# Performance work log

Hardware: AMD Instinct MI355X
Metric: run time of the kernel (lower is better)

Reference implementation:

```python
import jax, jax.numpy as jnp
import numpy as np

H = 32          # query heads
HKV = 8         # kv heads
HD = 128        # head dim
BS = 64         # sparse block size
LOCAL = 16      # local blocks
VERT = 8        # vertical stride
STEP = 1        # head sliding step = max(1, VERT // H) for non-homo heads
BASE = 1000000.0
ROPE_SCALE = 1.0
SCALE = 1.0 / np.sqrt(HD)


def setup_inputs() -> dict:
    key = jax.random.key(0)
    ks = jax.random.split(key, 6)
    T, D = 2048, H * HD
    std = 0.02
    return {
        'hidden_states': jax.random.normal(ks[0], (T, D), jnp.float32),
        'positions': jnp.arange(T, dtype=jnp.int32),
        'Wq': jax.random.normal(ks[1], (D, H * HD), jnp.float32) * std,
        'bq': jnp.zeros((H * HD,), jnp.float32),
        'Wk': jax.random.normal(ks[2], (D, HKV * HD), jnp.float32) * std,
        'bk': jnp.zeros((HKV * HD,), jnp.float32),
        'Wv': jax.random.normal(ks[3], (D, HKV * HD), jnp.float32) * std,
        'bv': jnp.zeros((HKV * HD,), jnp.float32),
        'Wo': jax.random.normal(ks[4], (D, D), jnp.float32) * std,
        'bo': jnp.zeros((D,), jnp.float32),
    }


def _rope_cos_sin(positions):
    # neox-style rotary, linear scaling (factor 1.0 -> identity)
    inv_freq = 1.0 / (BASE ** (jnp.arange(0, HD, 2, dtype=jnp.float32) / HD))  # [HD/2]
    t = positions.astype(jnp.float32) / ROPE_SCALE                             # [T]
    freqs = t[:, None] * inv_freq[None, :]                                     # [T, HD/2]
    return jnp.cos(freqs), jnp.sin(freqs)


def _apply_rope(x, cos, sin):
    # x: [T, h, HD], neox: rotate halves
    x1, x2 = x[..., : HD // 2], x[..., HD // 2 :]
    c, s = cos[:, None, :], sin[:, None, :]
    return jnp.concatenate([x1 * c - x2 * s, x2 * c + x1 * s], axis=-1)


def _block_sparse_mask(T):
    # per-head local + vertical-stride block pattern, causal at token level
    blk = jnp.arange(T) // BS
    qb, kb = blk[:, None], blk[None, :]                      # [T,T] block ids
    heads = jnp.arange(H)
    local = (qb - kb) < LOCAL                                # [T,T]
    vert = ((kb[None, :, :] + heads[:, None, None] * STEP + 1) % VERT) == 0  # [H,T,T]
    causal = jnp.arange(T)[:, None] >= jnp.arange(T)[None, :]
    return causal[None] & (local[None] | vert)               # [H,T,T] bool


def reference(hidden_states, positions, Wq, bq, Wk, bk, Wv, bv, Wo, bo):
    T = hidden_states.shape[0]
    q = (hidden_states @ Wq + bq).reshape(T, H, HD)
    k = (hidden_states @ Wk + bk).reshape(T, HKV, HD)
    v = (hidden_states @ Wv + bv).reshape(T, HKV, HD)

    cos, sin = _rope_cos_sin(positions)
    q = _apply_rope(q, cos, sin)
    k = _apply_rope(k, cos, sin)

    # GQA: repeat kv heads to match query heads
    k = jnp.repeat(k, H // HKV, axis=1)   # [T,H,HD]
    v = jnp.repeat(v, H // HKV, axis=1)

    scores = jnp.einsum('shd,thd->hst', q, k) * SCALE         # [H,T,T]
    mask = _block_sparse_mask(T)
    scores = jnp.where(mask, scores, jnp.finfo(scores.dtype).min)
    probs = jax.nn.softmax(scores, axis=-1)
    out = jnp.einsum('hst,thd->shd', probs, v).reshape(T, H * HD)
    return out @ Wo + bo
```

## Files before the change

### kernel.cpp

```cpp
#include <hip/hip_runtime.h>
#include <type_traits>

#define H_    32
#define HKV_  8
#define HD_   128
#define D_    4096
#define KVD_  1024
#define NQKV_ 6144

typedef __attribute__((ext_vector_type(8))) short s8v;
typedef __attribute__((ext_vector_type(4))) float f4v;

__device__ __forceinline__ float b2f(unsigned short u) {
  union { unsigned int i; float f; } v; v.i = ((unsigned int)u) << 16; return v.f;
}
__device__ __forceinline__ unsigned short f2b(float f) {
  unsigned int u = __float_as_uint(f);
  u += 0x7fffu + ((u >> 16) & 1u);
  return (unsigned short)(u >> 16);
}

__device__ __forceinline__ void gload16(const unsigned short* g, unsigned short* l) {
  __builtin_amdgcn_global_load_lds((const __attribute__((address_space(1))) void*)g,
                                   (__attribute__((address_space(3))) void*)l, 16, 0, 0);
}

__global__ void cvt_bf16(const float* __restrict__ x, unsigned short* __restrict__ y,
                         int n8)
{
  int i = blockIdx.x * blockDim.x + threadIdx.x;
  if (i >= n8) return;
  const float4* xp = (const float4*)x + (size_t)i * 2;
  float4 a = xp[0], b = xp[1];
  s8v v;
  v[0] = (short)f2b(a.x); v[1] = (short)f2b(a.y);
  v[2] = (short)f2b(a.z); v[3] = (short)f2b(a.w);
  v[4] = (short)f2b(b.x); v[5] = (short)f2b(b.y);
  v[6] = (short)f2b(b.z); v[7] = (short)f2b(b.w);
  *(s8v*)(y + (size_t)i * 8) = v;
}

__global__ void concat_bias(const float* __restrict__ bq, const float* __restrict__ bk,
                            const float* __restrict__ bv, float* __restrict__ o)
{
  int i = blockIdx.x * blockDim.x + threadIdx.x;
  float v = (i < D_) ? bq[i] : (i < D_ + KVD_) ? bk[i - D_] : bv[i - D_ - KVD_];
  o[i] = v;
}

__global__ __launch_bounds__(256) void cvt_transpose(
    const float* __restrict__ W, unsigned short* __restrict__ Wt, int K, int N)
{
  __shared__ unsigned short tile[64][72];
  const int k0 = blockIdx.y * 64, n0 = blockIdx.x * 64;
  const int tid = threadIdx.x;
#pragma unroll
  for (int it = 0; it < 4; ++it) {
    int idx = tid + it * 256;
    int r = idx >> 4;
    int c = (idx & 15) << 2;
    float4 w = *(const float4*)(W + (size_t)(k0 + r) * N + n0 + c);
    tile[c + 0][r] = f2b(w.x); tile[c + 1][r] = f2b(w.y);
    tile[c + 2][r] = f2b(w.z); tile[c + 3][r] = f2b(w.w);
  }
  __syncthreads();
#pragma unroll
  for (int it = 0; it < 2; ++it) {
    int idx = tid + it * 256;
    int n = idx >> 3;
    int kk = (idx & 7) << 3;
    *(s8v*)(Wt + (size_t)(n0 + n) * K + k0 + kk) = *(const s8v*)&tile[n][kk];
  }
}

__global__ __launch_bounds__(256) void vtrans(
    const unsigned short* __restrict__ S, int lds_, unsigned short* __restrict__ Dst,
    int T)
{
  __shared__ unsigned short tile[64][72];
  const int v0 = blockIdx.x * 64, t0 = blockIdx.y * 64;
  const int tid = threadIdx.x;
#pragma unroll
  for (int it = 0; it < 2; ++it) {
    int idx = tid + it * 256;
    int tr = idx >> 3;
    int vc = (idx & 7) << 3;
    s8v val = *(const s8v*)(S + (size_t)(t0 + tr) * lds_ + v0 + vc);
#pragma unroll
    for (int u = 0; u < 8; ++u) tile[vc + u][tr] = (unsigned short)val[u];
  }
  __syncthreads();
#pragma unroll
  for (int it = 0; it < 2; ++it) {
    int idx = tid + it * 256;
    int vr = idx >> 3;
    int tc = (idx & 7) << 3;
    *(s8v*)(Dst + (size_t)(v0 + vr) * T + t0 + tc) = *(const s8v*)&tile[vr][tc];
  }
}

template <typename OT>
__global__ __launch_bounds__(512, 2) void gemm_bt8(
    const unsigned short* __restrict__ A, const unsigned short* __restrict__ Bt,
    const float* __restrict__ bias, OT* __restrict__ C,
    int M, int N, int K, int ldc)
{
  __shared__ __align__(16) unsigned short lds[65536];

  const int tid  = threadIdx.x;
  const int wave = tid >> 6;
  const int lane = tid & 63;
  const int l16  = lane & 15;
  const int quad = lane >> 4;
  const int wm   = wave >> 2;
  const int wn   = wave & 3;

  const int nbx = N >> 8;
  const int nwg = nbx * (M >> 8);
  int bid = blockIdx.x;
  if ((nwg & 7) == 0) bid = (bid & 7) * (nwg >> 3) + (bid >> 3);
  const int row0 = (bid / nbx) << 8;
  const int col0 = (bid % nbx) << 8;

  const int srow = lane >> 2;
  const int scol = ((lane & 3) ^ (srow & 3)) << 3;
  const unsigned short* Ap0 = A  + (size_t)(row0 + wave * 32 + srow) * K + scol;
  const unsigned short* Bp0 = Bt + (size_t)(col0 + wave * 32 + srow) * K + scol;

  auto STAGE_A = [&](int tile) {
    unsigned short* d = lds + (tile & 3) * 8192 + wave * 1024;
    const unsigned short* s = Ap0 + (size_t)tile * 32;
    gload16(s, d);
    gload16(s + 16 * (size_t)K, d + 512);
  };
  auto STAGE_B = [&](int tile) {
    unsigned short* d = lds + 32768 + (tile & 3) * 8192 + wave * 1024;
    const unsigned short* s = Bp0 + (size_t)tile * 32;
    gload16(s, d);
    gload16(s + 16 * (size_t)K, d + 512);
  };

  const int slot = ((quad ^ (l16 & 3)) << 3);
  const int aoff = (wm * 128 + l16) * 32 + slot;
  const int boff = (wn * 64  + l16) * 32 + slot;

  f4v acc[8][4] = {};
  const int nt = K >> 5;

  STAGE_A(0); STAGE_B(0);
  STAGE_A(1); STAGE_B(1);
  STAGE_A(2); STAGE_B(2);
  asm volatile("s_waitcnt vmcnt(8)" ::: "memory");
  __builtin_amdgcn_s_barrier();

  for (int t = 0; t < nt; ++t) {
    const unsigned short* Ab = lds + (t & 3) * 8192;
    const unsigned short* Bb = lds + 32768 + (t & 3) * 8192;
    s8v a[8], b[4];

    if (t + 3 < nt) STAGE_A(t + 3);
#pragma unroll
    for (int i = 0; i < 4; ++i) a[i] = *(const s8v*)&Ab[aoff + i * 512];
#pragma unroll
    for (int j = 0; j < 4; ++j) b[j] = *(const s8v*)&Bb[boff + j * 512];
    __builtin_amdgcn_s_barrier();
    asm volatile("s_waitcnt lgkmcnt(0)" ::: "memory");
    __builtin_amdgcn_sched_barrier(0);
    __builtin_amdgcn_s_setprio(1);
#pragma unroll
    for (int i = 0; i < 4; ++i)
#pragma unroll
      for (int j = 0; j < 4; ++j)
        acc[i][j] = __builtin_amdgcn_mfma_f32_16x16x32_bf16(a[i], b[j], acc[i][j], 0, 0, 0);
    __builtin_amdgcn_s_setprio(0);
    __builtin_amdgcn_s_barrier();

    if (t + 3 < nt) STAGE_B(t + 3);
#pragma unroll
    for (int i = 0; i < 4; ++i) a[4 + i] = *(const s8v*)&Ab[aoff + (4 + i) * 512];
    __builtin_amdgcn_s_barrier();
    asm volatile("s_waitcnt lgkmcnt(0)" ::: "memory");
    __builtin_amdgcn_sched_barrier(0);
    __builtin_amdgcn_s_setprio(1);
#pragma unroll
    for (int i = 0; i < 4; ++i)
#pragma unroll
      for (int j = 0; j < 4; ++j)
        acc[4 + i][j] = __builtin_amdgcn_mfma_f32_16x16x32_bf16(a[4 + i], b[j], acc[4 + i][j], 0, 0, 0);
    __builtin_amdgcn_s_setprio(0);
    if (t < nt - 3)       { asm volatile("s_waitcnt vmcnt(8)" ::: "memory"); }
    else if (t == nt - 3) { asm volatile("s_waitcnt vmcnt(4)" ::: "memory"); }
    else if (t == nt - 2) { asm volatile("s_waitcnt vmcnt(0)" ::: "memory"); }
    __builtin_amdgcn_s_barrier();
  }

#pragma unroll
  for (int j = 0; j < 4; ++j) {
    const int col = col0 + wn * 64 + j * 16 + l16;
    const float bc = bias[col];
#pragma unroll
    for (int i = 0; i < 8; ++i) {
      const int rowb = row0 + wm * 128 + i * 16 + quad * 4;
#pragma unroll
      for (int r = 0; r < 4; ++r) {
        float o = acc[i][j][r] + bc;
        if constexpr (std::is_same_v<OT, float>) C[(size_t)(rowb + r) * ldc + col] = o;
        else                                     C[(size_t)(rowb + r) * ldc + col] = f2b(o);
      }
    }
  }
}

__global__ __launch_bounds__(256) void gemm_bt2(
    const unsigned short* __restrict__ A, const unsigned short* __restrict__ Bt,
    const float* __restrict__ bias, float* __restrict__ C, int M, int N, int K)
{
  __shared__ __align__(16) unsigned short As[128 * 32];
  __shared__ __align__(16) unsigned short Bs[64 * 32];

  const int tid  = threadIdx.x;
  const int wave = tid >> 6;
  const int lane = tid & 63;
  const int l16  = lane & 15;
  const int quad = lane >> 4;
  const int row0 = blockIdx.y * 128;
  const int col0 = blockIdx.x * 64;
  const int wr   = wave >> 1, wc = wave & 1;

  const int srow = lane >> 2;
  const int skk  = (lane & 3) << 3;
  const unsigned short* Ap = A  + (size_t)(row0 + wave * 32 + srow) * K + skk;
  const unsigned short* Bp = Bt + (size_t)(col0 + wave * 16 + srow) * K + skk;
  unsigned short* AsW = As + wave * 1024;
  unsigned short* BsW = Bs + wave * 512;

  f4v acc[4][2] = {};

  for (int k0 = 0; k0 < K; k0 += 32) {
    __syncthreads();
    gload16(Ap,           AsW);
    gload16(Ap + 16 * K,  AsW + 512);
    gload16(Bp,           BsW);
    Ap += 32; Bp += 32;
    __syncthreads();

    s8v a[4], b[2];
#pragma unroll
    for (int i = 0; i < 4; ++i)
      a[i] = *(const s8v*)&As[(wr * 64 + i * 16 + l16) * 32 + quad * 8];
#pragma unroll
    for (int j = 0; j < 2; ++j)
      b[j] = *(const s8v*)&Bs[(wc * 32 + j * 16 + l16) * 32 + quad * 8];
#pragma unroll
    for (int i = 0; i < 4; ++i)
#pragma unroll
      for (int j = 0; j < 2; ++j)
        acc[i][j] = __builtin_amdgcn_mfma_f32_16x16x32_bf16(a[i], b[j], acc[i][j], 0, 0, 0);
  }

#pragma unroll
  for (int j = 0; j < 2; ++j) {
    int col = col0 + wc * 32 + j * 16 + l16;
    float bc = bias[col];
#pragma unroll
    for (int i = 0; i < 4; ++i) {
#pragma unroll
      for (int r = 0; r < 4; ++r) {
        int row = row0 + wr * 64 + i * 16 + quad * 4 + r;
        C[(size_t)row * N + col] = acc[i][j][r] + bc;
      }
    }
  }
}

__global__ void sincos_tab(const int* __restrict__ pos, float* __restrict__ ct,
                           float* __restrict__ st)
{
  const int t = blockIdx.x, d = threadIdx.x;
  float inv = powf(1.0e6f, -(float)d * (1.0f / 64.0f));
  float fr  = (float)pos[t] * inv;
  float s, c;
  sincosf(fr, &s, &c);
  ct[t * 64 + d] = c;
  st[t * 64 + d] = s;
}

__global__ void rope_apply(unsigned short* __restrict__ qkv,
                           const float* __restrict__ ct, const float* __restrict__ st,
                           int T)
{
  const int t  = blockIdx.x;
  const int hh = blockIdx.y;
  const int d  = threadIdx.x;
  unsigned short* p = qkv + (size_t)t * NQKV_ + hh * HD_;
  const float g = (hh < H_) ? (0.08838834764831845f * 1.4426950408889634f) : 1.0f;
  float c = ct[t * 64 + d], s = st[t * 64 + d];
  float x1 = b2f(p[d]), x2 = b2f(p[d + 64]);
  p[d]      = f2b((x1 * c - x2 * s) * g);
  p[d + 64] = f2b((x2 * c + x1 * s) * g);
}

__global__ __launch_bounds__(256) void attn_sparse(
    const unsigned short* __restrict__ QKV, int ldq,
    const unsigned short* __restrict__ Vt, unsigned short* __restrict__ O, int T)
{
  __shared__ __align__(16) unsigned short lds[16384];
  unsigned short* ldsK = lds;
  unsigned short* ldsV = lds + 8192;
  unsigned short* ldsP = lds;

  const int h    = blockIdx.x;
  const int qb   = (gridDim.y - 1) - blockIdx.y;
  const int hkv  = h >> 2;
  const int tid  = threadIdx.x;
  const int wave = tid >> 6;
  const int lane = tid & 63;
  const int l16  = lane & 15;
  const int quad = lane >> 4;

  const int qrow = qb * 64 + wave * 16 + l16;
  s8v qf[4];
#pragma unroll
  for (int s = 0; s < 4; ++s)
    qf[s] = *(const s8v*)(QKV + (size_t)qrow * ldq + h * HD_ + s * 32 + quad * 8);

  const int lr4 = lane >> 2;
  const int lc8 = (lane & 3) << 3;
  const unsigned short* Kp0 = QKV + (size_t)(wave * 16 + lr4) * ldq
                              + D_ + hkv * HD_ + lc8;
  unsigned short* Kd0 = ldsK + wave * 512;
  const unsigned short* Vp0 = Vt + (size_t)(hkv * HD_ + wave * 32 + lr4) * T + lc8;
  unsigned short* Vd0 = ldsV + wave * 1024;

  float mrow[4] = {-1e30f, -1e30f, -1e30f, -1e30f};
  float lrow[4] = {0.f, 0.f, 0.f, 0.f};
  f4v oacc[8] = {};
  const int rowinb = wave * 16 + quad * 4;

  for (int kb = 0; kb <= qb; ++kb) {
    if (!((qb - kb < 16) || (((kb + h + 1) & 7) == 0))) continue;

    __syncthreads();
    {
      const unsigned short* kp = Kp0 + (size_t)(kb * 64) * ldq;
      const unsigned short* vp = Vp0 + kb * 64;
#pragma unroll
      for (int t = 0; t < 4; ++t)
        gload16(kp + t * 32, Kd0 + t * 2048);
#pragma unroll
      for (int t = 0; t < 4; ++t)
        gload16(vp + (size_t)((t >> 1) * 16) * T + (t & 1) * 32,
                Vd0 + (t & 1) * 4096 + (t >> 1) * 512);
    }
    __syncthreads();

    f4v sacc[4] = {};
#pragma unroll
    for (int kt = 0; kt < 4; ++kt) {
#pragma unroll
      for (int s = 0; s < 4; ++s) {
        s8v b = *(const s8v*)&ldsK[s * 2048 + (kt * 16 + l16) * 32 + quad * 8];
        sacc[kt] = __builtin_amdgcn_mfma_f32_16x16x32_bf16(qf[s], b, sacc[kt], 0, 0, 0);
      }
    }
    __syncthreads();

    const bool diag = (kb == qb);
    float p[4][4];
#pragma unroll
    for (int r = 0; r < 4; ++r) {
      float mx = -1e30f;
#pragma unroll
      for (int kt = 0; kt < 4; ++kt) {
        float sc = sacc[kt][r];
        if (diag && (kt * 16 + l16 > rowinb + r)) sc = -1e30f;
        p[r][kt] = sc;
        mx = fmaxf(mx, sc);
      }
#pragma unroll
      for (int off = 1; off < 16; off <<= 1)
        mx = fmaxf(mx, __shfl_xor(mx, off));
      float newm = fmaxf(mrow[r], mx);
      float alpha = exp2f(mrow[r] - newm);
      mrow[r] = newm;
      float rs = 0.f;
#pragma unroll
      for (int kt = 0; kt < 4; ++kt) {
        unsigned short pb = f2b(exp2f(p[r][kt] - newm));
        ldsP[wave * 1152 + (quad * 4 + r) * 72 + kt * 16 + l16] = pb;
        rs += b2f(pb);
      }
#pragma unroll
      for (int off = 1; off < 16; off <<= 1)
        rs += __shfl_xor(rs, off);
      lrow[r] = lrow[r] * alpha + rs;
#pragma unroll
      for (int dt = 0; dt < 8; ++dt) oacc[dt][r] *= alpha;
    }

#pragma unroll
    for (int s2 = 0; s2 < 2; ++s2) {
      s8v af = *(const s8v*)&ldsP[wave * 1152 + l16 * 72 + s2 * 32 + quad * 8];
#pragma unroll
      for (int dt = 0; dt < 8; ++dt) {
        s8v vf = *(const s8v*)&ldsV[s2 * 4096 + (dt * 16 + l16) * 32 + quad * 8];
        oacc[dt] = __builtin_amdgcn_mfma_f32_16x16x32_bf16(af, vf, oacc[dt], 0, 0, 0);
      }
    }
  }

#pragma unroll
  for (int r = 0; r < 4; ++r) {
    float inv = 1.0f / lrow[r];
    size_t rowoff = (size_t)(qb * 64 + rowinb + r) * D_ + h * HD_;
#pragma unroll
    for (int dt = 0; dt < 8; ++dt)
      O[rowoff + dt * 16 + l16] = f2b(oacc[dt][r] * inv);
  }
}

extern "C" void kernel_launch(void* const* d_in, const int* in_sizes, int n_in,
                              void* d_out, int out_size, void* d_ws, size_t ws_size,
                              hipStream_t stream)
{
  const float* hs  = (const float*)d_in[0];
  const int*   pos = (const int*)d_in[1];
  const float* Wq  = (const float*)d_in[2];
  const float* bq  = (const float*)d_in[3];
  const float* Wk  = (const float*)d_in[4];
  const float* bk  = (const float*)d_in[5];
  const float* Wv  = (const float*)d_in[6];
  const float* bv  = (const float*)d_in[7];
  const float* Wo  = (const float*)d_in[8];
  const float* bo  = (const float*)d_in[9];
  float* out = (float*)d_out;

  const int T = in_sizes[1];

  const size_t nQ = (size_t)T * D_;
  unsigned short* hsb  = (unsigned short*)d_ws;
  unsigned short* qkv  = hsb + nQ;
  unsigned short* vt   = qkv + (size_t)T * NQKV_;
  unsigned short* wbuf = vt  + (size_t)KVD_ * T;
  unsigned short* tail = wbuf + (size_t)NQKV_ * D_;
  float* bqkv = (float*)tail;
  float* ct   = bqkv + NQKV_;
  float* st   = ct + (size_t)T * 64;
  unsigned short* abuf = hsb;

  dim3 blk(256);
  cvt_bf16<<<dim3((int)(nQ / 8 / 256)), blk, 0, stream>>>(hs, hsb, (int)(nQ / 8));
  concat_bias<<<dim3(NQKV_ / 256), blk, 0, stream>>>(bq, bk, bv, bqkv);
  sincos_tab<<<dim3(T), dim3(64), 0, stream>>>(pos, ct, st);

  cvt_transpose<<<dim3(D_ / 64,   D_ / 64), blk, 0, stream>>>(Wq, wbuf, D_, D_);
  cvt_transpose<<<dim3(KVD_ / 64, D_ / 64), blk, 0, stream>>>(
      Wk, wbuf + (size_t)D_ * D_, D_, KVD_);
  cvt_transpose<<<dim3(KVD_ / 64, D_ / 64), blk, 0, stream>>>(
      Wv, wbuf + (size_t)(D_ + KVD_) * D_, D_, KVD_);

  gemm_bt8<unsigned short><<<dim3((NQKV_ / 256) * (T / 256)), dim3(512), 0, stream>>>(
      hsb, wbuf, bqkv, qkv, T, NQKV_, D_, NQKV_);

  rope_apply<<<dim3(T, H_ + HKV_), dim3(64), 0, stream>>>(qkv, ct, st, T);
  vtrans<<<dim3(KVD_ / 64, T / 64), blk, 0, stream>>>(
      qkv + D_ + KVD_, NQKV_, vt, T);

  attn_sparse<<<dim3(H_, T / 64), blk, 0, stream>>>(qkv, NQKV_, vt, abuf, T);

  cvt_transpose<<<dim3(D_ / 64, D_ / 64), blk, 0, stream>>>(Wo, wbuf, D_, D_);
  gemm_bt2<<<dim3(D_ / 64, T / 128), blk, 0, stream>>>(
      abuf, wbuf, bo, out, T, D_, D_);
}
```

Baseline: 560.7 us.

## Restructure big GEMM into double-buffered 64-K pipeline and reuse it for output projection

```diff
diff --git a/kernel.cpp b/kernel.cpp
--- a/kernel.cpp
+++ b/kernel.cpp
@@ -100,7 +100,7 @@
 }
 
 template <typename OT>
-__global__ __launch_bounds__(512, 2) void gemm_bt8(
+__global__ __launch_bounds__(512, 2) void gemm_bt4p(
     const unsigned short* __restrict__ A, const unsigned short* __restrict__ Bt,
     const float* __restrict__ bias, OT* __restrict__ C,
     int M, int N, int K, int ldc)
@@ -123,75 +123,117 @@
   const int col0 = (bid % nbx) << 8;
 
   const int srow = lane >> 2;
-  const int scol = ((lane & 3) ^ (srow & 3)) << 3;
-  const unsigned short* Ap0 = A  + (size_t)(row0 + wave * 32 + srow) * K + scol;
-  const unsigned short* Bp0 = Bt + (size_t)(col0 + wave * 32 + srow) * K + scol;
-
-  auto STAGE_A = [&](int tile) {
-    unsigned short* d = lds + (tile & 3) * 8192 + wave * 1024;
-    const unsigned short* s = Ap0 + (size_t)tile * 32;
-    gload16(s, d);
-    gload16(s + 16 * (size_t)K, d + 512);
-  };
-  auto STAGE_B = [&](int tile) {
-    unsigned short* d = lds + 32768 + (tile & 3) * 8192 + wave * 1024;
-    const unsigned short* s = Bp0 + (size_t)tile * 32;
-    gload16(s, d);
-    gload16(s + 16 * (size_t)K, d + 512);
-  };
-
-  const int slot = ((quad ^ (l16 & 3)) << 3);
-  const int aoff = (wm * 128 + l16) * 32 + slot;
-  const int boff = (wn * 64  + l16) * 32 + slot;
+  const int scol = (lane & 3) << 3;
+  const unsigned short* ApL = A  + (size_t)(row0 + wave * 32 + srow) * K + scol;
+  const unsigned short* BpL = Bt + (size_t)(col0 + wave * 32 + srow) * K + scol;
+
+  unsigned short* ldsA = lds;
+  unsigned short* ldsB = lds + 32768;
+  const int wst = wave * 1024;
 
   f4v acc[8][4] = {};
-  const int nt = K >> 5;
-
-  STAGE_A(0); STAGE_B(0);
-  STAGE_A(1); STAGE_B(1);
-  STAGE_A(2); STAGE_B(2);
-  asm volatile("s_waitcnt vmcnt(8)" ::: "memory");
-  __builtin_amdgcn_s_barrier();
+  const int nt = K >> 6;
+
+  {
+    const unsigned short* sa = ApL;
+    const unsigned short* sb = BpL;
+    gload16(sa,                      ldsA + wst);
+    gload16(sa + 16 * (size_t)K,     ldsA + wst + 512);
+    gload16(sb,                      ldsB + wst);
+    gload16(sb + 16 * (size_t)K,     ldsB + wst + 512);
+    gload16(sa + 32,                 ldsA + 8192 + wst);
+    gload16(sa + 32 + 16 * (size_t)K, ldsA + 8192 + wst + 512);
+    gload16(sb + 32,                 ldsB + 8192 + wst);
+    gload16(sb + 32 + 16 * (size_t)K, ldsB + 8192 + wst + 512);
+  }
 
   for (int t = 0; t < nt; ++t) {
-    const unsigned short* Ab = lds + (t & 3) * 8192;
-    const unsigned short* Bb = lds + 32768 + (t & 3) * 8192;
+    const int p  = t & 1;
+    const unsigned short* Ab = ldsA + p * 16384;
+    const unsigned short* Bb = ldsB + p * 16384;
+    unsigned short* An = ldsA + (p ^ 1) * 16384;
+    unsigned short* Bn = ldsB + (p ^ 1) * 16384;
+    const bool pre = (t + 1 < nt);
+    const unsigned short* sa = ApL + (size_t)(t + 1) * 64;
+    const unsigned short* sb = BpL + (size_t)(t + 1) * 64;
+
     s8v a[8], b[4];
 
-    if (t + 3 < nt) STAGE_A(t + 3);
-#pragma unroll
-    for (int i = 0; i < 4; ++i) a[i] = *(const s8v*)&Ab[aoff + i * 512];
-#pragma unroll
-    for (int j = 0; j < 4; ++j) b[j] = *(const s8v*)&Bb[boff + j * 512];
+    if (pre) {
+      gload16(sa,                  An + wst);
+      gload16(sa + 16 * (size_t)K, An + wst + 512);
+      asm volatile("s_waitcnt vmcnt(6)" ::: "memory");
+    } else {
+      asm volatile("s_waitcnt vmcnt(4)" ::: "memory");
+    }
     __builtin_amdgcn_s_barrier();
-    asm volatile("s_waitcnt lgkmcnt(0)" ::: "memory");
+    __builtin_amdgcn_sched_barrier(0);
+    b[0] = *(const s8v*)&Bb[(wn * 64 +  0 + l16) * 32 + quad * 8];
+    b[1] = *(const s8v*)&Bb[(wn * 64 + 16 + l16) * 32 + quad * 8];
+#pragma unroll
+    for (int i = 0; i < 8; ++i)
+      a[i] = *(const s8v*)&Ab[(wm * 128 + i * 16 + l16) * 32 + quad * 8];
+    __builtin_amdgcn_s_setprio(1);
+#pragma unroll
+    for (int i = 0; i < 8; ++i) {
+      acc[i][0] = __builtin_amdgcn_mfma_f32_16x16x32_bf16(a[i], b[0], acc[i][0], 0, 0, 0);
+      acc[i][1] = __builtin_amdgcn_mfma_f32_16x16x32_bf16(a[i], b[1], acc[i][1], 0, 0, 0);
+    }
+    __builtin_amdgcn_s_setprio(0);
+
+    if (pre) {
+      gload16(sb,                  Bn + wst);
+      gload16(sb + 16 * (size_t)K, Bn + wst + 512);
+    }
+    b[2] = *(const s8v*)&Bb[(wn * 64 + 32 + l16) * 32 + quad * 8];
+    b[3] = *(const s8v*)&Bb[(wn * 64 + 48 + l16) * 32 + quad * 8];
+    __builtin_amdgcn_s_barrier();
     __builtin_amdgcn_sched_barrier(0);
     __builtin_amdgcn_s_setprio(1);
 #pragma unroll
-    for (int i = 0; i < 4; ++i)
-#pragma unroll
-      for (int j = 0; j < 4; ++j)
-        acc[i][j] = __builtin_amdgcn_mfma_f32_16x16x32_bf16(a[i], b[j], acc[i][j], 0, 0, 0);
+    for (int i = 0; i < 8; ++i) {
+      acc[i][2] = __builtin_amdgcn_mfma_f32_16x16x32_bf16(a[i], b[2], acc[i][2], 0, 0, 0);
+      acc[i][3] = __builtin_amdgcn_mfma_f32_16x16x32_bf16(a[i], b[3], acc[i][3], 0, 0, 0);
+    }
     __builtin_amdgcn_s_setprio(0);
+
+    if (pre) {
+      gload16(sa + 32,                  An + 8192 + wst);
+      gload16(sa + 32 + 16 * (size_t)K, An + 8192 + wst + 512);
+      asm volatile("s_waitcnt vmcnt(6)" ::: "memory");
+    } else {
+      asm volatile("s_waitcnt vmcnt(0)" ::: "memory");
+    }
     __builtin_amdgcn_s_barrier();
-
-    if (t + 3 < nt) STAGE_B(t + 3);
-#pragma unroll
-    for (int i = 0; i < 4; ++i) a[4 + i] = *(const s8v*)&Ab[aoff + (4 + i) * 512];
+    __builtin_amdgcn_sched_barrier(0);
+    b[2] = *(const s8v*)&Bb[8192 + (wn * 64 + 32 + l16) * 32 + quad * 8];
+    b[3] = *(const s8v*)&Bb[8192 + (wn * 64 + 48 + l16) * 32 + quad * 8];
+#pragma unroll
+    for (int i = 0; i < 8; ++i)
+      a[i] = *(const s8v*)&Ab[8192 + (wm * 128 + i * 16 + l16) * 32 + quad * 8];
+    __builtin_amdgcn_s_setprio(1);
+#pragma unroll
+    for (int i = 0; i < 8; ++i) {
+      acc[i][2] = __builtin_amdgcn_mfma_f32_16x16x32_bf16(a[i], b[2], acc[i][2], 0, 0, 0);
+      acc[i][3] = __builtin_amdgcn_mfma_f32_16x16x32_bf16(a[i], b[3], acc[i][3], 0, 0, 0);
+    }
+    __builtin_amdgcn_s_setprio(0);
+
+    if (pre) {
+      gload16(sb + 32,                  Bn + 8192 + wst);
+      gload16(sb + 32 + 16 * (size_t)K, Bn + 8192 + wst + 512);
+    }
+    b[0] = *(const s8v*)&Bb[8192 + (wn * 64 +  0 + l16) * 32 + quad * 8];
+    b[1] = *(const s8v*)&Bb[8192 + (wn * 64 + 16 + l16) * 32 + quad * 8];
     __builtin_amdgcn_s_barrier();
-    asm volatile("s_waitcnt lgkmcnt(0)" ::: "memory");
     __builtin_amdgcn_sched_barrier(0);
     __builtin_amdgcn_s_setprio(1);
 #pragma unroll
-    for (int i = 0; i < 4; ++i)
-#pragma unroll
-      for (int j = 0; j < 4; ++j)
-        acc[4 + i][j] = __builtin_amdgcn_mfma_f32_16x16x32_bf16(a[4 + i], b[j], acc[4 + i][j], 0, 0, 0);
+    for (int i = 0; i < 8; ++i) {
+      acc[i][0] = __builtin_amdgcn_mfma_f32_16x16x32_bf16(a[i], b[0], acc[i][0], 0, 0, 0);
+      acc[i][1] = __builtin_amdgcn_mfma_f32_16x16x32_bf16(a[i], b[1], acc[i][1], 0, 0, 0);
+    }
     __builtin_amdgcn_s_setprio(0);
-    if (t < nt - 3)       { asm volatile("s_waitcnt vmcnt(8)" ::: "memory"); }
-    else if (t == nt - 3) { asm volatile("s_waitcnt vmcnt(4)" ::: "memory"); }
-    else if (t == nt - 2) { asm volatile("s_waitcnt vmcnt(0)" ::: "memory"); }
-    __builtin_amdgcn_s_barrier();
   }
 
 #pragma unroll
@@ -206,68 +248,6 @@
         float o = acc[i][j][r] + bc;
         if constexpr (std::is_same_v<OT, float>) C[(size_t)(rowb + r) * ldc + col] = o;
         else                                     C[(size_t)(rowb + r) * ldc + col] = f2b(o);
-      }
-    }
-  }
-}
-
-__global__ __launch_bounds__(256) void gemm_bt2(
-    const unsigned short* __restrict__ A, const unsigned short* __restrict__ Bt,
-    const float* __restrict__ bias, float* __restrict__ C, int M, int N, int K)
-{
-  __shared__ __align__(16) unsigned short As[128 * 32];
-  __shared__ __align__(16) unsigned short Bs[64 * 32];
-
-  const int tid  = threadIdx.x;
-  const int wave = tid >> 6;
-  const int lane = tid & 63;
-  const int l16  = lane & 15;
-  const int quad = lane >> 4;
-  const int row0 = blockIdx.y * 128;
-  const int col0 = blockIdx.x * 64;
-  const int wr   = wave >> 1, wc = wave & 1;
-
-  const int srow = lane >> 2;
-  const int skk  = (lane & 3) << 3;
-  const unsigned short* Ap = A  + (size_t)(row0 + wave * 32 + srow) * K + skk;
-  const unsigned short* Bp = Bt + (size_t)(col0 + wave * 16 + srow) * K + skk;
-  unsigned short* AsW = As + wave * 1024;
-  unsigned short* BsW = Bs + wave * 512;
-
-  f4v acc[4][2] = {};
-
-  for (int k0 = 0; k0 < K; k0 += 32) {
-    __syncthreads();
-    gload16(Ap,           AsW);
-    gload16(Ap + 16 * K,  AsW + 512);
-    gload16(Bp,           BsW);
-    Ap += 32; Bp += 32;
-    __syncthreads();
-
-    s8v a[4], b[2];
-#pragma unroll
-    for (int i = 0; i < 4; ++i)
-      a[i] = *(const s8v*)&As[(wr * 64 + i * 16 + l16) * 32 + quad * 8];
-#pragma unroll
-    for (int j = 0; j < 2; ++j)
-      b[j] = *(const s8v*)&Bs[(wc * 32 + j * 16 + l16) * 32 + quad * 8];
-#pragma unroll
-    for (int i = 0; i < 4; ++i)
-#pragma unroll
-      for (int j = 0; j < 2; ++j)
-        acc[i][j] = __builtin_amdgcn_mfma_f32_16x16x32_bf16(a[i], b[j], acc[i][j], 0, 0, 0);
-  }
-
-#pragma unroll
-  for (int j = 0; j < 2; ++j) {
-    int col = col0 + wc * 32 + j * 16 + l16;
-    float bc = bias[col];
-#pragma unroll
-    for (int i = 0; i < 4; ++i) {
-#pragma unroll
-      for (int r = 0; r < 4; ++r) {
-        int row = row0 + wr * 64 + i * 16 + quad * 4 + r;
-        C[(size_t)row * N + col] = acc[i][j][r] + bc;
       }
     }
   }
@@ -459,7 +439,7 @@
   cvt_transpose<<<dim3(KVD_ / 64, D_ / 64), blk, 0, stream>>>(
       Wv, wbuf + (size_t)(D_ + KVD_) * D_, D_, KVD_);
 
-  gemm_bt8<unsigned short><<<dim3((NQKV_ / 256) * (T / 256)), dim3(512), 0, stream>>>(
+  gemm_bt4p<unsigned short><<<dim3((NQKV_ / 256) * (T / 256)), dim3(512), 0, stream>>>(
       hsb, wbuf, bqkv, qkv, T, NQKV_, D_, NQKV_);
 
   rope_apply<<<dim3(T, H_ + HKV_), dim3(64), 0, stream>>>(qkv, ct, st, T);
@@ -469,6 +449,6 @@
   attn_sparse<<<dim3(H_, T / 64), blk, 0, stream>>>(qkv, NQKV_, vt, abuf, T);
 
   cvt_transpose<<<dim3(D_ / 64, D_ / 64), blk, 0, stream>>>(Wo, wbuf, D_, D_);
-  gemm_bt2<<<dim3(D_ / 64, T / 128), blk, 0, stream>>>(
-      abuf, wbuf, bo, out, T, D_, D_);
-}
+  gemm_bt4p<float><<<dim3((D_ / 256) * (T / 256)), dim3(512), 0, stream>>>(
+      abuf, wbuf, bo, out, T, D_, D_, D_);
+}
```

Result: no change. 558.4 us (-0.4%).
